# Kernel tuning notes

Measured on AMD Instinct MI355X. Metric: run time of the kernel, lower is better.

Reference implementation:

```python
import jax, jax.numpy as jnp
import numpy as np

REPR_OUT = (16, 16, 16)   # multiplicities for l=0,1,2
STRIDE = 2                # GatedBlock stride with smooth_stride=True -> low-pass+stride after gate
PAD = 2                   # conv padding
C_IN = 72                 # 8*1 + 8*3 + 8*5
C_OUT_GATED = 176         # 144 fields + 32 gate scalars
KSIZE = 5


def conv3d(x, w, stride, padding):
    return jax.lax.conv_general_dilated(
        x, w, window_strides=(stride,) * 3,
        padding=[(padding, padding)] * 3,
        dimension_numbers=('NCDHW', 'OIDHW', 'NCDHW'))


def low_pass_filter(z, scale, stride):
    # gaussian blur (sigma from scale) applied depthwise, then strided -- as in se3cnn
    sigma = 0.5 * (scale ** 2 - 1) ** 0.5
    size = int(1 + 2 * 2.5 * sigma)
    if size % 2 == 0:
        size += 1
    r = np.arange(size) - size // 2
    g1 = np.exp(-r.astype(np.float64) ** 2 / (2 * sigma ** 2))
    g = g1[:, None, None] * g1[None, :, None] * g1[None, None, :]
    g = (g / g.sum()).astype(np.float32)
    B, C = z.shape[0], z.shape[1]
    zz = z.reshape(B * C, 1, *z.shape[2:])
    out = conv3d(zz, jnp.asarray(g)[None, None], stride, size // 2)
    return out.reshape(B, C, *out.shape[2:])


def gate(y, scalar_bias, gate_bias):
    # y: [B, 176, X, Y, Z]; split into 144 field channels + 32 gate scalars
    size_out = sum(mul * (2 * n + 1) for n, mul in enumerate(REPR_OUT))
    B, _, nx, ny, nz = y.shape
    g = jax.nn.sigmoid(y[:, size_out:] + gate_bias[None, :, None, None, None])
    fields = []
    begin_y, begin_g = 0, 0
    for n, mul in enumerate(REPR_OUT):
        if mul == 0:
            continue
        dim = 2 * n + 1
        fy = y[:, begin_y:begin_y + mul * dim]
        if n == 0:
            # scalar fields: bias + relu (ScalarActivation)
            fields.append(jax.nn.relu(fy + scalar_bias[None, :, None, None, None]))
        else:
            fg = g[:, begin_g:begin_g + mul]
            begin_g += mul
            f = fy.reshape(B, mul, dim, nx, ny, nz) * fg[:, :, None]  # broadcast gate over 2l+1
            fields.append(f.reshape(B, mul * dim, nx, ny, nz))
        begin_y += mul * dim
    return jnp.concatenate(fields, axis=1)  # [B, 144, X, Y, Z]


def setup_inputs() -> dict:
    key = jax.random.key(0)
    k1, k2, k3, k4 = jax.random.split(key, 4)
    fan_in = C_IN * KSIZE ** 3
    x = jax.random.normal(k1, (4, C_IN, 32, 32, 32), dtype=jnp.float32)
    W = jax.random.normal(k2, (C_OUT_GATED, C_IN, KSIZE, KSIZE, KSIZE), dtype=jnp.float32) / np.sqrt(fan_in)
    scalar_bias = jax.random.normal(k3, (REPR_OUT[0],), dtype=jnp.float32) * 0.1
    gate_bias = jax.random.normal(k4, (sum(REPR_OUT[1:]),), dtype=jnp.float32) * 0.1
    return {'x': x, 'W': W, 'scalar_bias': scalar_bias, 'gate_bias': gate_bias}


def reference(x, W, scalar_bias, gate_bias):
    y = conv3d(x, W, 1, PAD)                 # SE3 conv at stride 1 (smooth_stride)
    z = gate(y, scalar_bias, gate_bias)      # per-irrep gated nonlinearity
    z = low_pass_filter(z, STRIDE, STRIDE)   # gaussian low-pass + stride 2
    return z
```

## Files before the change

### kernel.cpp

```cpp
#include <hip/hip_runtime.h>
#include <cstdint>
#include <cstddef>

typedef short short8 __attribute__((ext_vector_type(8)));
typedef float floatx4 __attribute__((ext_vector_type(4)));
typedef unsigned short u16;

__device__ __forceinline__ u16 f2bf(float f) {
    unsigned u = __float_as_uint(f);
    u += 0x7FFFu + ((u >> 16) & 1u);
    return (u16)(u >> 16);
}
__device__ __forceinline__ float bf2f(u16 h) {
    return __uint_as_float(((unsigned)h) << 16);
}

__device__ __forceinline__ void gload_lds16(const u16* g, u16* l) {
    __builtin_amdgcn_global_load_lds(
        (const __attribute__((address_space(1))) void*)g,
        (__attribute__((address_space(3))) void*)l, 16, 0, 0);
}

__global__ __launch_bounds__(256) void k_transpose_x(const float* __restrict__ x,
                                                     u16* __restrict__ xt) {
    __shared__ float tile[72 * 33];
    const int bx = blockIdx.x;
    const int tid = threadIdx.x;
    const int b = bx >> 10, d = (bx >> 5) & 31, h = bx & 31;
    const float* src = x + (size_t)b * 72 * 32768 + d * 1024 + h * 32;
    for (int e = tid; e < 2304; e += 256) {
        int ci = e >> 5, w = e & 31;
        tile[ci * 33 + w] = src[(size_t)ci * 32768 + w];
    }
    __syncthreads();
    u16* dst = xt + (size_t)bx * 2304;
    for (int e = tid; e < 2304; e += 256) {
        int w = e / 72, ci = e - w * 72;
        dst[e] = f2bf(tile[ci * 33 + w]);
    }
}

__global__ __launch_bounds__(256) void k_prep_w(const float* __restrict__ W,
                                                u16* __restrict__ wt) {
    const int gid = blockIdx.x * 256 + threadIdx.x;
    const int frag = gid >> 6, lane = gid & 63;
    const int nb = frag % 11;
    int t = frag / 11;
    const int kb = t % 12;
    t = t / 12;
    const int kh = t % 5, kd = t / 5;
    const int n = lane & 15, q8 = (lane >> 4) * 8;
    const int co = nb * 16 + n;
    u16 v[8] __attribute__((aligned(16)));
    #pragma unroll
    for (int j = 0; j < 8; ++j) {
        int k = kb * 32 + q8 + j;
        u16 r = 0;
        if (k < 360) {
            int kw = k / 72, ci = k - kw * 72;
            r = f2bf(W[((size_t)co * 72 + ci) * 125 + kd * 25 + kh * 5 + kw]);
        }
        v[j] = r;
    }
    *(uint4*)(wt + (size_t)gid * 8) = *(const uint4*)v;
}

#define LP 2624
#define MFMA_BF16 __builtin_amdgcn_mfma_f32_16x16x32_bf16

#define STAGE_PAIR(s0_) do {                                                       \
    _Pragma("unroll")                                                              \
    for (int cc = 0; cc < 3; ++cc) {                                               \
        const int c_  = wv + cc * 8;                                               \
        const int st_ = (s0_) + (c_ >= 11 ? 1 : 0);                                \
        const int nb_ = (c_ >= 11) ? (c_ - 11) : c_;                               \
        if (c_ < 22 && st_ < 60)                                                   \
            gload_lds16(wt_kd + (size_t)st_ * 5632 + nb_ * 512 + lane * 8,         \
                        sB + (st_ & 3) * 5632 + nb_ * 512);                        \
    }                                                                              \
} while (0)

#define CSTEP(aoff_, buf_) do {                                                    \
    const u16* ap_ = sxA + (aoff_);                                                \
    short8 A0_ = *(const short8*)(ap_);                                            \
    short8 A1_ = *(const short8*)(ap_ + 1152);                                     \
    short8 A2_ = *(const short8*)(ap_ + LP);                                       \
    short8 A3_ = *(const short8*)(ap_ + LP + 1152);                                \
    const u16* bb_ = sB + (buf_) * 5632 + lane * 8;                                \
    _Pragma("unroll")                                                              \
    for (int j = 0; j < 11; ++j) {                                                 \
        short8 bv = *(const short8*)(bb_ + j * 512);                               \
        acc[0][j] = MFMA_BF16(A0_, bv, acc[0][j], 0, 0, 0);                        \
        acc[1][j] = MFMA_BF16(A1_, bv, acc[1][j], 0, 0, 0);                        \
        acc[2][j] = MFMA_BF16(A2_, bv, acc[2][j], 0, 0, 0);                        \
        acc[3][j] = MFMA_BF16(A3_, bv, acc[3][j], 0, 0, 0);                        \
    }                                                                              \
} while (0)

__global__ __launch_bounds__(512, 2) void k_conv(const u16* __restrict__ xt,
                                                 const u16* __restrict__ wt,
                                                 const float* __restrict__ scalar_bias,
                                                 const float* __restrict__ gate_bias,
                                                 u16* __restrict__ zt) {
    __shared__ __align__(16) u16 sx[20 * LP];
    __shared__ __align__(16) u16 sB[4 * 5632];
    const int bx = blockIdx.x;
    const int swz = (bx & 7) * 32 + (bx >> 3);
    const int ht = swz & 1, d = (swz >> 1) & 31, b = swz >> 6;
    const int h0 = ht * 16;
    const int tid = threadIdx.x, lane = tid & 63, wv = tid >> 6;
    const int c15 = lane & 15, q = lane >> 4;

    floatx4 acc[4][11];
    #pragma unroll
    for (int i = 0; i < 4; ++i) {
        #pragma unroll
        for (int j = 0; j < 11; ++j) acc[i][j] = (floatx4){0.f, 0.f, 0.f, 0.f};
    }

    const int laneA = c15 * 72 + q * 8;
    const u16* sxA = &sx[2 * wv * LP + laneA];

    for (int kd = 0; kd < 5; ++kd) {
        const int dp = d + kd - 2;
        if (dp < 0 || dp >= 32) continue;
        const u16* wt_kd = wt + (size_t)kd * 5 * 67584;

        __syncthreads();
        const u16* srcbase = xt + (size_t)((b * 32 + dp) * 32) * 2304;
        for (int idx = tid; idx < 20 * 328; idx += 512) {
            int r = idx / 328, c = idx - r * 328;
            int hp = h0 + r - 2;
            uint4 val = make_uint4(0u, 0u, 0u, 0u);
            if (hp >= 0 && hp < 32 && c >= 18 && c < 306)
                val = *(const uint4*)(srcbase + (size_t)hp * 2304 + (c * 8 - 144));
            *(uint4*)(&sx[r * LP + c * 8]) = val;
        }
        STAGE_PAIR(0);
        __syncthreads();

        int kh = 0, kb = 0;
        #pragma unroll 1
        for (int kp = 0; kp < 60; kp += 2) {
            if (kp) __syncthreads();
            STAGE_PAIR(kp + 2);
            const int aoff = kh * LP + kb * 32;
            CSTEP(aoff,      kp & 3);
            CSTEP(aoff + 32, (kp + 1) & 3);
            kb += 2;
            if (kb == 12) { kb = 0; ++kh; }
        }
    }

    const float sb = scalar_bias[c15];
    int   slA[9];
    float gbA[9];
    #pragma unroll
    for (int nb = 1; nb <= 8; ++nb) {
        int idx = (nb - 1) * 16 + c15;
        int mul = (nb <= 3) ? (idx / 3) : (16 + (idx - 48) / 5);
        slA[nb] = (lane & 48) | (mul & 15);
        gbA[nb] = gate_bias[mul];
    }
    #pragma unroll
    for (int mi = 0; mi < 4; ++mi) {
        const int hl = 2 * wv + (mi >> 1);
        const int wh = mi & 1;
        const size_t zrow0 = (size_t)((b * 32 + d) * 32 + (h0 + hl)) * 32;
        #pragma unroll
        for (int r = 0; r < 4; ++r) {
            const int w = wh * 16 + q * 4 + r;
            u16* zp = zt + (zrow0 + w) * 144;
            zp[c15] = f2bf(fmaxf(acc[mi][0][r] + sb, 0.f));
            const float g9v  = acc[mi][9][r];
            const float g10v = acc[mi][10][r];
            #pragma unroll
            for (int nb = 1; nb <= 8; ++nb) {
                float ys = __shfl((nb <= 3) ? g9v : g10v, slA[nb], 64);
                float g  = 1.f / (1.f + __expf(-(ys + gbA[nb])));
                zp[nb * 16 + c15] = f2bf(acc[mi][nb][r] * g);
            }
        }
    }
}

__global__ __launch_bounds__(256) void k_lowpass_dh(const u16* __restrict__ zt,
                                                    float* __restrict__ tmp) {
    const int gid = blockIdx.x * 256 + threadIdx.x;
    const int c8 = gid % 18;
    int r = gid / 18;
    const int w  = r & 31; r >>= 5;
    const int oh = r & 15; r >>= 4;
    const int od = r & 15; r >>= 4;
    const int b  = r;
    const float lw[5] = {0.03208210f, 0.23705644f, 0.46172277f, 0.23705644f, 0.03208210f};
    float a[8];
    #pragma unroll
    for (int j = 0; j < 8; ++j) a[j] = 0.f;
    for (int kd = 0; kd < 5; ++kd) {
        const int dz = 2 * od + kd - 2;
        if (dz < 0 || dz >= 32) continue;
        for (int kh = 0; kh < 5; ++kh) {
            const int hz = 2 * oh + kh - 2;
            if (hz < 0 || hz >= 32) continue;
            const float wt2 = lw[kd] * lw[kh];
            const u16* p = zt + ((size_t)((b * 32 + dz) * 32 + hz) * 32 + w) * 144 + c8 * 8;
            u16 v[8] __attribute__((aligned(16)));
            *(uint4*)v = *(const uint4*)p;
            #pragma unroll
            for (int j = 0; j < 8; ++j) a[j] += wt2 * bf2f(v[j]);
        }
    }
    float* tp = tmp + ((size_t)(((b * 16 + od) * 16 + oh) * 32) + w) * 144 + c8 * 8;
    *(float4*)(tp)     = make_float4(a[0], a[1], a[2], a[3]);
    *(float4*)(tp + 4) = make_float4(a[4], a[5], a[6], a[7]);
}

__global__ __launch_bounds__(256) void k_lowpass_w(const float* __restrict__ tmp,
                                                   float* __restrict__ out) {
    const int gid = blockIdx.x * 256 + threadIdx.x;
    const int c8 = gid % 18;
    int r = gid / 18;
    const int ow = r & 15; r >>= 4;
    const int oh = r & 15; r >>= 4;
    const int od = r & 15; r >>= 4;
    const int b  = r;
    const float lw[5] = {0.03208210f, 0.23705644f, 0.46172277f, 0.23705644f, 0.03208210f};
    float a[8];
    #pragma unroll
    for (int j = 0; j < 8; ++j) a[j] = 0.f;
    const float* tb = tmp + ((size_t)(((b * 16 + od) * 16 + oh) * 32)) * 144 + c8 * 8;
    #pragma unroll
    for (int kw = 0; kw < 5; ++kw) {
        const int wz = 2 * ow + kw - 2;
        if (wz < 0 || wz >= 32) continue;
        const float wt1 = lw[kw];
        const float* p = tb + (size_t)wz * 144;
        float4 v0 = *(const float4*)(p);
        float4 v1 = *(const float4*)(p + 4);
        a[0] += wt1 * v0.x; a[1] += wt1 * v0.y; a[2] += wt1 * v0.z; a[3] += wt1 * v0.w;
        a[4] += wt1 * v1.x; a[5] += wt1 * v1.y; a[6] += wt1 * v1.z; a[7] += wt1 * v1.w;
    }
    const int c0 = c8 * 8;
    float* op = out + ((size_t)b * 144 + c0) * 4096 + od * 256 + oh * 16 + ow;
    #pragma unroll
    for (int j = 0; j < 8; ++j) op[(size_t)j * 4096] = a[j];
}

extern "C" void kernel_launch(void* const* d_in, const int* in_sizes, int n_in,
                              void* d_out, int out_size, void* d_ws, size_t ws_size,
                              hipStream_t stream) {
    const float* x  = (const float*)d_in[0];
    const float* W  = (const float*)d_in[1];
    const float* sb = (const float*)d_in[2];
    const float* gb = (const float*)d_in[3];
    float* out = (float*)d_out;

    char* ws = (char*)d_ws;
    u16* xt = (u16*)(ws);
    u16* wt = (u16*)(ws + 18874368);
    u16* zt = (u16*)(ws + 22253568);
    float* tmp = (float*)(ws);

    hipLaunchKernelGGL(k_transpose_x, dim3(4096), dim3(256), 0, stream, x, xt);
    hipLaunchKernelGGL(k_prep_w,      dim3(825),  dim3(256), 0, stream, W, wt);
    hipLaunchKernelGGL(k_conv,        dim3(256),  dim3(512), 0, stream, xt, wt, sb, gb, zt);
    hipLaunchKernelGGL(k_lowpass_dh,  dim3(2304), dim3(256), 0, stream, zt, tmp);
    hipLaunchKernelGGL(k_lowpass_w,   dim3(1152), dim3(256), 0, stream, tmp, out);
}
```

Baseline: 479.3 us.

## Shrink conv block to 8 rows, double-buffer 9 weight tiles, read rest from global

The conv kernel now uses 256-thread blocks covering 8 output rows instead of 16, launching twice as many blocks. The weight staging moves from a 4-slot, two-k-step pipeline to a 2-slot single-step double buffer holding 9 of the 11 output-channel tiles. The other two tiles are loaded straight from global memory, and the MFMA section is wrapped in s_setprio. The point is to cut LDS footprint and raise occupancy or block count for better CU fill. In exchange it reloads more input halo per block, adds more barriers, and adds direct global loads that sit on the MFMA critical path.

```diff
diff --git a/kernel.cpp b/kernel.cpp
--- a/kernel.cpp
+++ b/kernel.cpp
@@ -65,49 +65,29 @@
     *(uint4*)(wt + (size_t)gid * 8) = *(const uint4*)v;
 }
 
-#define LP 2624
+#define LP 2592
 #define MFMA_BF16 __builtin_amdgcn_mfma_f32_16x16x32_bf16
 
-#define STAGE_PAIR(s0_) do {                                                       \
-    _Pragma("unroll")                                                              \
-    for (int cc = 0; cc < 3; ++cc) {                                               \
-        const int c_  = wv + cc * 8;                                               \
-        const int st_ = (s0_) + (c_ >= 11 ? 1 : 0);                                \
-        const int nb_ = (c_ >= 11) ? (c_ - 11) : c_;                               \
-        if (c_ < 22 && st_ < 60)                                                   \
-            gload_lds16(wt_kd + (size_t)st_ * 5632 + nb_ * 512 + lane * 8,         \
-                        sB + (st_ & 3) * 5632 + nb_ * 512);                        \
-    }                                                                              \
+#define STAGE(kk_, slot_) do {                                                     \
+    const u16* gs_ = wt_kd + (size_t)(kk_) * 5632 + lane * 8;                      \
+    u16* ds_ = sB + (slot_) * 4608;                                                \
+    gload_lds16(gs_ + wv * 512, ds_ + wv * 512);                                   \
+    gload_lds16(gs_ + (wv + 4) * 512, ds_ + (wv + 4) * 512);                       \
+    if (wv == 0) gload_lds16(gs_ + 8 * 512, ds_ + 8 * 512);                        \
 } while (0)
 
-#define CSTEP(aoff_, buf_) do {                                                    \
-    const u16* ap_ = sxA + (aoff_);                                                \
-    short8 A0_ = *(const short8*)(ap_);                                            \
-    short8 A1_ = *(const short8*)(ap_ + 1152);                                     \
-    short8 A2_ = *(const short8*)(ap_ + LP);                                       \
-    short8 A3_ = *(const short8*)(ap_ + LP + 1152);                                \
-    const u16* bb_ = sB + (buf_) * 5632 + lane * 8;                                \
-    _Pragma("unroll")                                                              \
-    for (int j = 0; j < 11; ++j) {                                                 \
-        short8 bv = *(const short8*)(bb_ + j * 512);                               \
-        acc[0][j] = MFMA_BF16(A0_, bv, acc[0][j], 0, 0, 0);                        \
-        acc[1][j] = MFMA_BF16(A1_, bv, acc[1][j], 0, 0, 0);                        \
-        acc[2][j] = MFMA_BF16(A2_, bv, acc[2][j], 0, 0, 0);                        \
-        acc[3][j] = MFMA_BF16(A3_, bv, acc[3][j], 0, 0, 0);                        \
-    }                                                                              \
-} while (0)
-
-__global__ __launch_bounds__(512, 2) void k_conv(const u16* __restrict__ xt,
+__global__ __launch_bounds__(256, 2) void k_conv(const u16* __restrict__ xt,
                                                  const u16* __restrict__ wt,
                                                  const float* __restrict__ scalar_bias,
                                                  const float* __restrict__ gate_bias,
                                                  u16* __restrict__ zt) {
-    __shared__ __align__(16) u16 sx[20 * LP];
-    __shared__ __align__(16) u16 sB[4 * 5632];
+    __shared__ __align__(16) u16 smem[12 * LP + 2 * 4608];
+    u16* sx = smem;
+    u16* sB = smem + 12 * LP;
     const int bx = blockIdx.x;
-    const int swz = (bx & 7) * 32 + (bx >> 3);
-    const int ht = swz & 1, d = (swz >> 1) & 31, b = swz >> 6;
-    const int h0 = ht * 16;
+    const int swz = (bx & 7) * 64 + (bx >> 3);
+    const int ht = swz & 3, d = (swz >> 2) & 31, b = swz >> 7;
+    const int h0 = ht * 8;
     const int tid = threadIdx.x, lane = tid & 63, wv = tid >> 6;
     const int c15 = lane & 15, q = lane >> 4;
 
@@ -119,7 +99,7 @@
     }
 
     const int laneA = c15 * 72 + q * 8;
-    const u16* sxA = &sx[2 * wv * LP + laneA];
+    const u16* sxA = sx + 2 * wv * LP + laneA;
 
     for (int kd = 0; kd < 5; ++kd) {
         const int dp = d + kd - 2;
@@ -128,27 +108,50 @@
 
         __syncthreads();
         const u16* srcbase = xt + (size_t)((b * 32 + dp) * 32) * 2304;
-        for (int idx = tid; idx < 20 * 328; idx += 512) {
-            int r = idx / 328, c = idx - r * 328;
+        for (int idx = tid; idx < 12 * 324; idx += 256) {
+            int r = idx / 324, c = idx - r * 324;
             int hp = h0 + r - 2;
             uint4 val = make_uint4(0u, 0u, 0u, 0u);
             if (hp >= 0 && hp < 32 && c >= 18 && c < 306)
                 val = *(const uint4*)(srcbase + (size_t)hp * 2304 + (c * 8 - 144));
             *(uint4*)(&sx[r * LP + c * 8]) = val;
         }
-        STAGE_PAIR(0);
+        STAGE(0, 0);
         __syncthreads();
 
         int kh = 0, kb = 0;
         #pragma unroll 1
-        for (int kp = 0; kp < 60; kp += 2) {
-            if (kp) __syncthreads();
-            STAGE_PAIR(kp + 2);
-            const int aoff = kh * LP + kb * 32;
-            CSTEP(aoff,      kp & 3);
-            CSTEP(aoff + 32, (kp + 1) & 3);
-            kb += 2;
-            if (kb == 12) { kb = 0; ++kh; }
+        for (int kk = 0; kk < 60; ++kk) {
+            if (kk) __syncthreads();
+            if (kk < 59) STAGE(kk + 1, (kk + 1) & 1);
+            const u16* gB_ = wt_kd + (size_t)kk * 5632 + lane * 8;
+            short8 B9  = *(const short8*)(gB_ + 9 * 512);
+            short8 B10 = *(const short8*)(gB_ + 10 * 512);
+            const u16* ap = sxA + kh * LP + kb * 32;
+            short8 A0 = *(const short8*)(ap);
+            short8 A1 = *(const short8*)(ap + 1152);
+            short8 A2 = *(const short8*)(ap + LP);
+            short8 A3 = *(const short8*)(ap + LP + 1152);
+            const u16* bb = sB + (kk & 1) * 4608 + lane * 8;
+            __builtin_amdgcn_s_setprio(1);
+            #pragma unroll
+            for (int j = 0; j < 9; ++j) {
+                short8 bv = *(const short8*)(bb + j * 512);
+                acc[0][j] = MFMA_BF16(A0, bv, acc[0][j], 0, 0, 0);
+                acc[1][j] = MFMA_BF16(A1, bv, acc[1][j], 0, 0, 0);
+                acc[2][j] = MFMA_BF16(A2, bv, acc[2][j], 0, 0, 0);
+                acc[3][j] = MFMA_BF16(A3, bv, acc[3][j], 0, 0, 0);
+            }
+            acc[0][9]  = MFMA_BF16(A0, B9,  acc[0][9],  0, 0, 0);
+            acc[1][9]  = MFMA_BF16(A1, B9,  acc[1][9],  0, 0, 0);
+            acc[2][9]  = MFMA_BF16(A2, B9,  acc[2][9],  0, 0, 0);
+            acc[3][9]  = MFMA_BF16(A3, B9,  acc[3][9],  0, 0, 0);
+            acc[0][10] = MFMA_BF16(A0, B10, acc[0][10], 0, 0, 0);
+            acc[1][10] = MFMA_BF16(A1, B10, acc[1][10], 0, 0, 0);
+            acc[2][10] = MFMA_BF16(A2, B10, acc[2][10], 0, 0, 0);
+            acc[3][10] = MFMA_BF16(A3, B10, acc[3][10], 0, 0, 0);
+            __builtin_amdgcn_s_setprio(0);
+            if (++kb == 12) { kb = 0; ++kh; }
         }
     }
 
@@ -264,7 +267,7 @@
 
     hipLaunchKernelGGL(k_transpose_x, dim3(4096), dim3(256), 0, stream, x, xt);
     hipLaunchKernelGGL(k_prep_w,      dim3(825),  dim3(256), 0, stream, W, wt);
-    hipLaunchKernelGGL(k_conv,        dim3(256),  dim3(512), 0, stream, xt, wt, sb, gb, zt);
+    hipLaunchKernelGGL(k_conv,        dim3(512),  dim3(256), 0, stream, xt, wt, sb, gb, zt);
     hipLaunchKernelGGL(k_lowpass_dh,  dim3(2304), dim3(256), 0, stream, zt, tmp);
     hipLaunchKernelGGL(k_lowpass_w,   dim3(1152), dim3(256), 0, stream, tmp, out);
 }
```

Result: faster. 465.9 us (-2.8%).
